# Kernel optimization log

Measured on AMD Instinct MI355X. Metric: run time of the kernel, lower is better.

The kernel has to match this reference:

```python
import jax, jax.numpy as jnp
import numpy as np

N = 100000
E = 1600000
IN_FEATS = 128
OUT_FEATS = 64


def setup_inputs() -> dict:
    key = jax.random.key(0)
    ks = jax.random.split(key, 8)
    node_feat = jax.random.normal(ks[0], (N, IN_FEATS), dtype=jnp.float32)
    edge_feat = jax.random.normal(ks[1], (E, 1), dtype=jnp.float32)
    # Linear params (PyTorch Linear: y = x @ W^T + b; we store W already transposed as [in, out])
    W_node = jax.random.normal(ks[2], (IN_FEATS, OUT_FEATS), dtype=jnp.float32) / np.sqrt(IN_FEATS)
    b_node = jax.random.normal(ks[3], (OUT_FEATS,), dtype=jnp.float32) * 0.01
    W_edge = jax.random.normal(ks[4], (1, OUT_FEATS), dtype=jnp.float32)
    b_edge = jax.random.normal(ks[5], (OUT_FEATS,), dtype=jnp.float32) * 0.01
    src = jax.random.randint(ks[6], (E,), 0, N, dtype=jnp.int32)
    dst = jax.random.randint(ks[7], (E,), 0, N, dtype=jnp.int32)
    return {"node_feat": node_feat, "edge_feat": edge_feat, "W_node": W_node,
            "b_node": b_node, "W_edge": W_edge, "b_edge": b_edge,
            "src": src, "dst": dst}


def reference(node_feat, edge_feat, W_node, b_node, W_edge, b_edge, src, dst):
    n_nodes = node_feat.shape[0]
    # node linear: h = node_fc(node_feat)  -> [N, out]
    h = node_feat @ W_node + b_node
    # edge linear: he = edge_fc(edge_feat) -> [E, out]
    he = edge_feat @ W_edge + b_edge
    # u_add_e: m = h[src] + he  (gather + add)  -> [E, out]
    m = h[src] + he
    # mean aggregate over destination nodes (segment mean; 0 for isolated nodes, as in DGL)
    msg_sum = jax.ops.segment_sum(m, dst, num_segments=n_nodes)  # [N, out]
    deg = jax.ops.segment_sum(jnp.ones((dst.shape[0],), dtype=m.dtype), dst, num_segments=n_nodes)  # [N]
    h_new = msg_sum / jnp.maximum(deg, 1.0)[:, None]
    return h_new
```

## Files before the change

kernel.cpp:

```cpp
#include <hip/hip_runtime.h>

#define IN_F 128
#define OUT_F 64
#define BSH 6
#define BNODES 64
#define NBMAX 1600
#define MSC 6144
#define CAPB 2048

typedef __attribute__((ext_vector_type(8))) short short8;
typedef __attribute__((ext_vector_type(4))) float f32x4;

static __device__ __forceinline__ unsigned short f2bf(float f) {
    unsigned u = __float_as_uint(f);
    u += 0x7FFF + ((u >> 16) & 1);
    return (unsigned short)(u >> 16);
}

__global__ void prep(const float* __restrict__ W, unsigned short* __restrict__ Wt,
                     int* __restrict__ gcur, int nb) {
    int i = blockIdx.x * 256 + threadIdx.x;
    if (i < OUT_F * IN_F) {
        int o = i >> 7, k = i & 127;
        Wt[i] = f2bf(W[k * OUT_F + o]);
    }
    if (i < nb) gcur[i] = i * CAPB;
}

__global__ __launch_bounds__(256) void node_linear_mfma(const float* __restrict__ nf,
                                                        const unsigned short* __restrict__ Wt,
                                                        const float* __restrict__ bn,
                                                        unsigned short* __restrict__ h16,
                                                        int n_nodes, int n_tiles) {
    const int lane = threadIdx.x & 63;
    const int wid  = threadIdx.x >> 6;
    const int l15  = lane & 15;
    const int kq   = lane >> 4;

    short8 bfrag[4][4];
#pragma unroll
    for (int c = 0; c < 4; ++c)
#pragma unroll
        for (int ks = 0; ks < 4; ++ks)
            bfrag[c][ks] = *(const short8*)&Wt[(c * 16 + l15) * IN_F + ks * 32 + kq * 8];

    float bv[4];
#pragma unroll
    for (int c = 0; c < 4; ++c) bv[c] = bn[c * 16 + l15];

    for (int tile = blockIdx.x * 4 + wid; tile < n_tiles; tile += gridDim.x * 4) {
        int arow = tile * 16 + l15;
        if (arow >= n_nodes) arow = n_nodes - 1;
        const float* rp = nf + (size_t)arow * IN_F + kq * 8;

        f32x4 acc[4];
#pragma unroll
        for (int c = 0; c < 4; ++c) acc[c] = (f32x4){bv[c], bv[c], bv[c], bv[c]};

#pragma unroll
        for (int ks = 0; ks < 4; ++ks) {
            float4 x0 = *(const float4*)(rp + ks * 32);
            float4 x1 = *(const float4*)(rp + ks * 32 + 4);
            short8 af;
            af[0] = (short)f2bf(x0.x); af[1] = (short)f2bf(x0.y);
            af[2] = (short)f2bf(x0.z); af[3] = (short)f2bf(x0.w);
            af[4] = (short)f2bf(x1.x); af[5] = (short)f2bf(x1.y);
            af[6] = (short)f2bf(x1.z); af[7] = (short)f2bf(x1.w);
#pragma unroll
            for (int c = 0; c < 4; ++c)
                acc[c] = __builtin_amdgcn_mfma_f32_16x16x32_bf16(af, bfrag[c][ks], acc[c], 0, 0, 0);
        }

#pragma unroll
        for (int j = 0; j < 4; ++j) {
            int node = tile * 16 + kq * 4 + j;
            if (node < n_nodes) {
#pragma unroll
                for (int c = 0; c < 4; ++c)
                    h16[(size_t)node * OUT_F + c * 16 + l15] = f2bf(acc[c][j]);
            }
        }
    }
}

__global__ __launch_bounds__(1024) void multisplit(const int* __restrict__ src,
                                                   const int* __restrict__ dst,
                                                   const float* __restrict__ ef,
                                                   int* __restrict__ gcur,
                                                   int2* __restrict__ es,
                                                   int n_edges, int nb) {
    __shared__ int2 stage[MSC];
    __shared__ unsigned short sbuck[MSC];
    __shared__ int lhist[NBMAX];
    __shared__ int lbase[NBMAX];
    __shared__ int lcur[NBMAX];
    __shared__ int gbase[NBMAX];
    __shared__ int part[1024];

    const int t = threadIdx.x;
    const int cb = blockIdx.x * MSC;
    const int valid = min(MSC, n_edges - cb);
    if (valid <= 0) return;

    for (int i = t; i < nb; i += 1024) lhist[i] = 0;

    int   dr[6]; int sr[6]; float fr[6];
#pragma unroll
    for (int k = 0; k < 6; ++k) {
        int i = t + (k << 10);
        if (i < valid) { dr[k] = dst[cb + i]; sr[k] = src[cb + i]; fr[k] = ef[cb + i]; }
        else           { dr[k] = -1; sr[k] = 0; fr[k] = 0.f; }
    }
    __syncthreads();

#pragma unroll
    for (int k = 0; k < 6; ++k)
        if (dr[k] >= 0) atomicAdd(&lhist[dr[k] >> BSH], 1);
    __syncthreads();

    {
        const int b0 = t << 1;
        int v0 = (b0 < nb) ? lhist[b0] : 0;
        int v1 = (b0 + 1 < nb) ? lhist[b0 + 1] : 0;
        int s = v0 + v1;
        part[t] = s;
        __syncthreads();
        for (int off = 1; off < 1024; off <<= 1) {
            int x = (t >= off) ? part[t - off] : 0;
            __syncthreads();
            part[t] += x;
            __syncthreads();
        }
        int excl = part[t] - s;
        if (b0 < nb)     { lbase[b0] = excl;          lcur[b0] = excl; }
        if (b0 + 1 < nb) { lbase[b0 + 1] = excl + v0; lcur[b0 + 1] = excl + v0; }
    }
    __syncthreads();

    for (int b = t; b < nb; b += 1024) {
        int c = lhist[b];
        gbase[b] = c ? atomicAdd(&gcur[b], c) : 0;
    }
    __syncthreads();

#pragma unroll
    for (int k = 0; k < 6; ++k) {
        if (dr[k] >= 0) {
            int b = dr[k] >> BSH;
            int p = atomicAdd(&lcur[b], 1);
            int dl = dr[k] & (BNODES - 1);
            stage[p] = make_int2((dl << 17) | sr[k], __float_as_int(fr[k]));
            sbuck[p] = (unsigned short)b;
        }
    }
    __syncthreads();

    for (int i = t; i < valid; i += 1024) {
        int b = sbuck[i];
        int pos = gbase[b] + (i - lbase[b]);
        if (pos < (b + 1) * CAPB) es[pos] = stage[i];
    }
}

__global__ __launch_bounds__(512, 6) void aggregate(const unsigned short* __restrict__ h16,
                                                    const int2* __restrict__ es,
                                                    const int* __restrict__ gcur,
                                                    const float* __restrict__ We,
                                                    const float* __restrict__ be,
                                                    float* __restrict__ out, int n_nodes) {
    __shared__ int2 stage[CAPB];
    __shared__ int lhist[BNODES];
    __shared__ int lbase[BNODES];
    __shared__ int lcur[BNODES];
    __shared__ int sc[BNODES];

    const int t = threadIdx.x;
    const int bkt = blockIdx.x;
    const int s0 = bkt * CAPB;
    int cnt = gcur[bkt] - s0;
    if (cnt > CAPB) cnt = CAPB;

    if (t < BNODES) lhist[t] = 0;
    __syncthreads();

    int2 er[4];
#pragma unroll
    for (int k = 0; k < 4; ++k) {
        int i = t + (k << 9);
        if (i < cnt) er[k] = es[s0 + i];
    }
#pragma unroll
    for (int k = 0; k < 4; ++k) {
        int i = t + (k << 9);
        if (i < cnt) atomicAdd(&lhist[((unsigned)er[k].x) >> 17], 1);
    }
    __syncthreads();

    if (t < BNODES) sc[t] = lhist[t];
    __syncthreads();
    for (int off = 1; off < BNODES; off <<= 1) {
        int v = (t < BNODES && t >= off) ? sc[t - off] : 0;
        __syncthreads();
        if (t < BNODES) sc[t] += v;
        __syncthreads();
    }
    if (t < BNODES) { int e0 = sc[t] - lhist[t]; lbase[t] = e0; lcur[t] = e0; }
    __syncthreads();

#pragma unroll
    for (int k = 0; k < 4; ++k) {
        int i = t + (k << 9);
        if (i < cnt) {
            int b = ((unsigned)er[k].x) >> 17;
            int p = atomicAdd(&lcur[b], 1);
            stage[p] = er[k];
        }
    }
    __syncthreads();

    const int wid  = t >> 6;
    const int lane = t & 63;
    const int q    = lane >> 4;
    const int o4e  = (lane & 15) << 2;
    const float4 we4 = *(const float4*)&We[o4e];
    const float4 be4 = *(const float4*)&be[o4e];

#pragma unroll
    for (int p = 0; p < 4; ++p) {
        const int dlA = (wid << 3) + (p << 1);
        const int dlB = dlA + 1;
        const int jA = lbase[dlA], dgA = lhist[dlA];
        const int jB = lbase[dlB], dgB = lhist[dlB];
        float4 aA = make_float4(0.f, 0.f, 0.f, 0.f);
        float4 aB = make_float4(0.f, 0.f, 0.f, 0.f);
        float sxA = 0.f, sxB = 0.f;
        const int jm = dgA > dgB ? dgA : dgB;
        for (int j = 0; j < jm; j += 4) {
            int2 eA = make_int2(0, 0), eB = make_int2(0, 0);
            if (j + q < dgA) eA = stage[jA + j + q];
            if (j + q < dgB) eB = stage[jB + j + q];
            uint2 hA = make_uint2(0u, 0u), hB = make_uint2(0u, 0u);
            if (j + q < dgA) hA = *(const uint2*)&h16[((size_t)(eA.x & 0x1FFFF) << 6) + o4e];
            if (j + q < dgB) hB = *(const uint2*)&h16[((size_t)(eB.x & 0x1FFFF) << 6) + o4e];
            aA.x += __uint_as_float(hA.x << 16);
            aA.y += __uint_as_float(hA.x & 0xFFFF0000u);
            aA.z += __uint_as_float(hA.y << 16);
            aA.w += __uint_as_float(hA.y & 0xFFFF0000u);
            sxA  += __int_as_float(eA.y);
            aB.x += __uint_as_float(hB.x << 16);
            aB.y += __uint_as_float(hB.x & 0xFFFF0000u);
            aB.z += __uint_as_float(hB.y << 16);
            aB.w += __uint_as_float(hB.y & 0xFFFF0000u);
            sxB  += __int_as_float(eB.y);
        }
#define RED_(v) { v += __shfl_xor(v, 16, 64); v += __shfl_xor(v, 32, 64); }
        RED_(aA.x) RED_(aA.y) RED_(aA.z) RED_(aA.w) RED_(sxA)
        RED_(aB.x) RED_(aB.y) RED_(aB.z) RED_(aB.w) RED_(sxB)
#undef RED_
        if (q == 0) {
            int nodeA = (bkt << BSH) + dlA;
            if (nodeA < n_nodes) {
                float4 r = make_float4(0.f, 0.f, 0.f, 0.f);
                if (dgA > 0) {
                    float dgf = (float)dgA, inv = 1.f / dgf;
                    r.x = (aA.x + we4.x * sxA + dgf * be4.x) * inv;
                    r.y = (aA.y + we4.y * sxA + dgf * be4.y) * inv;
                    r.z = (aA.z + we4.z * sxA + dgf * be4.z) * inv;
                    r.w = (aA.w + we4.w * sxA + dgf * be4.w) * inv;
                }
                *(float4*)&out[((size_t)nodeA << 6) + o4e] = r;
            }
            int nodeB = (bkt << BSH) + dlB;
            if (nodeB < n_nodes) {
                float4 r = make_float4(0.f, 0.f, 0.f, 0.f);
                if (dgB > 0) {
                    float dgf = (float)dgB, inv = 1.f / dgf;
                    r.x = (aB.x + we4.x * sxB + dgf * be4.x) * inv;
                    r.y = (aB.y + we4.y * sxB + dgf * be4.y) * inv;
                    r.z = (aB.z + we4.z * sxB + dgf * be4.z) * inv;
                    r.w = (aB.w + we4.w * sxB + dgf * be4.w) * inv;
                }
                *(float4*)&out[((size_t)nodeB << 6) + o4e] = r;
            }
        }
    }
}

extern "C" void kernel_launch(void* const* d_in, const int* in_sizes, int n_in,
                              void* d_out, int out_size, void* d_ws, size_t ws_size,
                              hipStream_t stream) {
    const float* nf  = (const float*)d_in[0];
    const float* ef  = (const float*)d_in[1];
    const float* Wn  = (const float*)d_in[2];
    const float* bn  = (const float*)d_in[3];
    const float* We  = (const float*)d_in[4];
    const float* be  = (const float*)d_in[5];
    const int*   src = (const int*)d_in[6];
    const int*   dst = (const int*)d_in[7];
    float* out = (float*)d_out;

    const int n_nodes = in_sizes[0] / IN_F;
    const int n_edges = in_sizes[6];
    const int nb = (n_nodes + BNODES - 1) >> BSH;
    const int n_tiles = (n_nodes + 15) / 16;

    char* w = (char*)d_ws;
    unsigned short* h16 = (unsigned short*)w; w += (size_t)n_nodes * OUT_F * sizeof(unsigned short);
    int2* es  = (int2*)w; w += (size_t)nb * CAPB * sizeof(int2);
    int* gcur = (int*)w;  w += (size_t)NBMAX * sizeof(int);
    unsigned short* Wt = (unsigned short*)w; w += (size_t)OUT_F * IN_F * sizeof(unsigned short);

    prep<<<32, 256, 0, stream>>>(Wn, Wt, gcur, nb);
    node_linear_mfma<<<782, 256, 0, stream>>>(nf, Wt, bn, h16, n_nodes, n_tiles);
    multisplit<<<(n_edges + MSC - 1) / MSC, 1024, 0, stream>>>(src, dst, ef, gcur, es, n_edges, nb);
    aggregate<<<nb, 512, 0, stream>>>(h16, es, gcur, We, be, out, n_nodes);
}
```

Baseline: 87.43 us.

## Shrink multisplit chunk, per-wave histograms, 4-node ILP in aggregate

```diff
diff --git a/kernel.cpp b/kernel.cpp
--- a/kernel.cpp
+++ b/kernel.cpp
@@ -5,7 +5,7 @@
 #define BSH 6
 #define BNODES 64
 #define NBMAX 1600
-#define MSC 6144
+#define MSC 4096
 #define CAPB 2048
 
 typedef __attribute__((ext_vector_type(8))) short short8;
@@ -92,7 +92,6 @@
     __shared__ int2 stage[MSC];
     __shared__ unsigned short sbuck[MSC];
     __shared__ int lhist[NBMAX];
-    __shared__ int lbase[NBMAX];
     __shared__ int lcur[NBMAX];
     __shared__ int gbase[NBMAX];
     __shared__ int part[1024];
@@ -104,9 +103,9 @@
 
     for (int i = t; i < nb; i += 1024) lhist[i] = 0;
 
-    int   dr[6]; int sr[6]; float fr[6];
-#pragma unroll
-    for (int k = 0; k < 6; ++k) {
+    int   dr[4]; int sr[4]; float fr[4];
+#pragma unroll
+    for (int k = 0; k < 4; ++k) {
         int i = t + (k << 10);
         if (i < valid) { dr[k] = dst[cb + i]; sr[k] = src[cb + i]; fr[k] = ef[cb + i]; }
         else           { dr[k] = -1; sr[k] = 0; fr[k] = 0.f; }
@@ -114,7 +113,7 @@
     __syncthreads();
 
 #pragma unroll
-    for (int k = 0; k < 6; ++k)
+    for (int k = 0; k < 4; ++k)
         if (dr[k] >= 0) atomicAdd(&lhist[dr[k] >> BSH], 1);
     __syncthreads();
 
@@ -132,8 +131,8 @@
             __syncthreads();
         }
         int excl = part[t] - s;
-        if (b0 < nb)     { lbase[b0] = excl;          lcur[b0] = excl; }
-        if (b0 + 1 < nb) { lbase[b0 + 1] = excl + v0; lcur[b0 + 1] = excl + v0; }
+        if (b0 < nb)     lcur[b0] = excl;
+        if (b0 + 1 < nb) lcur[b0 + 1] = excl + v0;
     }
     __syncthreads();
 
@@ -144,7 +143,7 @@
     __syncthreads();
 
 #pragma unroll
-    for (int k = 0; k < 6; ++k) {
+    for (int k = 0; k < 4; ++k) {
         if (dr[k] >= 0) {
             int b = dr[k] >> BSH;
             int p = atomicAdd(&lcur[b], 1);
@@ -157,22 +156,22 @@
 
     for (int i = t; i < valid; i += 1024) {
         int b = sbuck[i];
-        int pos = gbase[b] + (i - lbase[b]);
+        int pos = gbase[b] + (i - (lcur[b] - lhist[b]));
         if (pos < (b + 1) * CAPB) es[pos] = stage[i];
     }
 }
 
-__global__ __launch_bounds__(512, 6) void aggregate(const unsigned short* __restrict__ h16,
+__global__ __launch_bounds__(512, 8) void aggregate(const unsigned short* __restrict__ h16,
                                                     const int2* __restrict__ es,
                                                     const int* __restrict__ gcur,
                                                     const float* __restrict__ We,
                                                     const float* __restrict__ be,
                                                     float* __restrict__ out, int n_nodes) {
     __shared__ int2 stage[CAPB];
+    __shared__ int lhist8[8][BNODES];
     __shared__ int lhist[BNODES];
     __shared__ int lbase[BNODES];
     __shared__ int lcur[BNODES];
-    __shared__ int sc[BNODES];
 
     const int t = threadIdx.x;
     const int bkt = blockIdx.x;
@@ -180,9 +179,10 @@
     int cnt = gcur[bkt] - s0;
     if (cnt > CAPB) cnt = CAPB;
 
-    if (t < BNODES) lhist[t] = 0;
-    __syncthreads();
-
+    ((int*)lhist8)[t] = 0;
+    __syncthreads();
+
+    const int wv = t >> 6;
     int2 er[4];
 #pragma unroll
     for (int k = 0; k < 4; ++k) {
@@ -192,19 +192,24 @@
 #pragma unroll
     for (int k = 0; k < 4; ++k) {
         int i = t + (k << 9);
-        if (i < cnt) atomicAdd(&lhist[((unsigned)er[k].x) >> 17], 1);
-    }
-    __syncthreads();
-
-    if (t < BNODES) sc[t] = lhist[t];
-    __syncthreads();
-    for (int off = 1; off < BNODES; off <<= 1) {
-        int v = (t < BNODES && t >= off) ? sc[t - off] : 0;
-        __syncthreads();
-        if (t < BNODES) sc[t] += v;
-        __syncthreads();
-    }
-    if (t < BNODES) { int e0 = sc[t] - lhist[t]; lbase[t] = e0; lcur[t] = e0; }
+        if (i < cnt) atomicAdd(&lhist8[wv][((unsigned)er[k].x) >> 17], 1);
+    }
+    __syncthreads();
+
+    if (t < BNODES) {
+        int v = 0;
+#pragma unroll
+        for (int w = 0; w < 8; ++w) v += lhist8[w][t];
+        lhist[t] = v;
+        int s = v;
+#pragma unroll
+        for (int off = 1; off < 64; off <<= 1) {
+            int x = __shfl_up(s, off, 64);
+            if (t >= off) s += x;
+        }
+        lbase[t] = s - v;
+        lcur[t]  = s - v;
+    }
     __syncthreads();
 
 #pragma unroll
@@ -218,7 +223,6 @@
     }
     __syncthreads();
 
-    const int wid  = t >> 6;
     const int lane = t & 63;
     const int q    = lane >> 4;
     const int o4e  = (lane & 15) << 2;
@@ -226,61 +230,59 @@
     const float4 be4 = *(const float4*)&be[o4e];
 
 #pragma unroll
-    for (int p = 0; p < 4; ++p) {
-        const int dlA = (wid << 3) + (p << 1);
-        const int dlB = dlA + 1;
-        const int jA = lbase[dlA], dgA = lhist[dlA];
-        const int jB = lbase[dlB], dgB = lhist[dlB];
-        float4 aA = make_float4(0.f, 0.f, 0.f, 0.f);
-        float4 aB = make_float4(0.f, 0.f, 0.f, 0.f);
-        float sxA = 0.f, sxB = 0.f;
-        const int jm = dgA > dgB ? dgA : dgB;
+    for (int g = 0; g < 2; ++g) {
+        const int dl0 = (wv << 3) + (g << 2);
+        int jb[4], dgv[4];
+#pragma unroll
+        for (int u = 0; u < 4; ++u) { jb[u] = lbase[dl0 + u]; dgv[u] = lhist[dl0 + u]; }
+        float4 ac[4];
+        float sx[4];
+#pragma unroll
+        for (int u = 0; u < 4; ++u) { ac[u] = make_float4(0.f, 0.f, 0.f, 0.f); sx[u] = 0.f; }
+        int jm = max(max(dgv[0], dgv[1]), max(dgv[2], dgv[3]));
+
         for (int j = 0; j < jm; j += 4) {
-            int2 eA = make_int2(0, 0), eB = make_int2(0, 0);
-            if (j + q < dgA) eA = stage[jA + j + q];
-            if (j + q < dgB) eB = stage[jB + j + q];
-            uint2 hA = make_uint2(0u, 0u), hB = make_uint2(0u, 0u);
-            if (j + q < dgA) hA = *(const uint2*)&h16[((size_t)(eA.x & 0x1FFFF) << 6) + o4e];
-            if (j + q < dgB) hB = *(const uint2*)&h16[((size_t)(eB.x & 0x1FFFF) << 6) + o4e];
-            aA.x += __uint_as_float(hA.x << 16);
-            aA.y += __uint_as_float(hA.x & 0xFFFF0000u);
-            aA.z += __uint_as_float(hA.y << 16);
-            aA.w += __uint_as_float(hA.y & 0xFFFF0000u);
-            sxA  += __int_as_float(eA.y);
-            aB.x += __uint_as_float(hB.x << 16);
-            aB.y += __uint_as_float(hB.x & 0xFFFF0000u);
-            aB.z += __uint_as_float(hB.y << 16);
-            aB.w += __uint_as_float(hB.y & 0xFFFF0000u);
-            sxB  += __int_as_float(eB.y);
-        }
+            int2 e[4];
+#pragma unroll
+            for (int u = 0; u < 4; ++u)
+                e[u] = (j + q < dgv[u]) ? stage[jb[u] + j + q] : make_int2(0, 0);
+            uint2 h[4];
+#pragma unroll
+            for (int u = 0; u < 4; ++u)
+                h[u] = (j + q < dgv[u]) ? *(const uint2*)&h16[((size_t)(e[u].x & 0x1FFFF) << 6) + o4e]
+                                        : make_uint2(0u, 0u);
+#pragma unroll
+            for (int u = 0; u < 4; ++u) {
+                ac[u].x += __uint_as_float(h[u].x << 16);
+                ac[u].y += __uint_as_float(h[u].x & 0xFFFF0000u);
+                ac[u].z += __uint_as_float(h[u].y << 16);
+                ac[u].w += __uint_as_float(h[u].y & 0xFFFF0000u);
+                sx[u]   += __int_as_float(e[u].y);
+            }
+        }
+
 #define RED_(v) { v += __shfl_xor(v, 16, 64); v += __shfl_xor(v, 32, 64); }
-        RED_(aA.x) RED_(aA.y) RED_(aA.z) RED_(aA.w) RED_(sxA)
-        RED_(aB.x) RED_(aB.y) RED_(aB.z) RED_(aB.w) RED_(sxB)
+#pragma unroll
+        for (int u = 0; u < 4; ++u) {
+            RED_(ac[u].x) RED_(ac[u].y) RED_(ac[u].z) RED_(ac[u].w) RED_(sx[u])
+        }
 #undef RED_
         if (q == 0) {
-            int nodeA = (bkt << BSH) + dlA;
-            if (nodeA < n_nodes) {
-                float4 r = make_float4(0.f, 0.f, 0.f, 0.f);
-                if (dgA > 0) {
-                    float dgf = (float)dgA, inv = 1.f / dgf;
-                    r.x = (aA.x + we4.x * sxA + dgf * be4.x) * inv;
-                    r.y = (aA.y + we4.y * sxA + dgf * be4.y) * inv;
-                    r.z = (aA.z + we4.z * sxA + dgf * be4.z) * inv;
-                    r.w = (aA.w + we4.w * sxA + dgf * be4.w) * inv;
+#pragma unroll
+            for (int u = 0; u < 4; ++u) {
+                int node = (bkt << BSH) + dl0 + u;
+                if (node < n_nodes) {
+                    float4 r = make_float4(0.f, 0.f, 0.f, 0.f);
+                    int dg = dgv[u];
+                    if (dg > 0) {
+                        float dgf = (float)dg, inv = 1.f / dgf;
+                        r.x = (ac[u].x + we4.x * sx[u] + dgf * be4.x) * inv;
+                        r.y = (ac[u].y + we4.y * sx[u] + dgf * be4.y) * inv;
+                        r.z = (ac[u].z + we4.z * sx[u] + dgf * be4.z) * inv;
+                        r.w = (ac[u].w + we4.w * sx[u] + dgf * be4.w) * inv;
+                    }
+                    *(float4*)&out[((size_t)node << 6) + o4e] = r;
                 }
-                *(float4*)&out[((size_t)nodeA << 6) + o4e] = r;
-            }
-            int nodeB = (bkt << BSH) + dlB;
-            if (nodeB < n_nodes) {
-                float4 r = make_float4(0.f, 0.f, 0.f, 0.f);
-                if (dgB > 0) {
-                    float dgf = (float)dgB, inv = 1.f / dgf;
-                    r.x = (aB.x + we4.x * sxB + dgf * be4.x) * inv;
-                    r.y = (aB.y + we4.y * sxB + dgf * be4.y) * inv;
-                    r.z = (aB.z + we4.z * sxB + dgf * be4.z) * inv;
-                    r.w = (aB.w + we4.w * sxB + dgf * be4.w) * inv;
-                }
-                *(float4*)&out[((size_t)nodeB << 6) + o4e] = r;
             }
         }
     }
```

Result: slower. 91.47 us (+4.6%).
